# Performance work log

Hardware: AMD Instinct MI355X
Metric: run time of the kernel (lower is better)

The kernel has to match this reference:

```python
import jax, jax.numpy as jnp
import numpy as np

EPS = 1e-06  # min_gamma_value

def spectral_function(eigvals):
    # reciprocal spectral function: f(lambda) = 1 / lambda (lambda >= EPS by construction)
    return 1.0 / eigvals

def setup_inputs() -> dict:
    key = jax.random.key(0)
    x = jax.random.normal(key, (4, 64, 16, 128, 128), dtype=jnp.float32)  # [B, C, K, H, W]
    return {"x": x}

def reference(x):
    # [B, C, K, H, W] -> [B, H, W, K, C]
    m = jnp.transpose(x, (0, 3, 4, 2, 1))
    K = m.shape[-2]
    # per-pixel KxK Gram matrix, regularized
    sym = jnp.einsum('bhwkc,bhwlc->bhwkl', m, m) + EPS * jnp.eye(K, dtype=m.dtype)
    eigvals, eigvecs = jnp.linalg.eigh(sym)          # eigvals [B,H,W,K], eigvecs [B,H,W,K,K]
    f = spectral_function(eigvals)                    # elementwise spectral map
    # V diag(f) V^T
    out = jnp.einsum('bhwik,bhwk,bhwjk->bhwij', eigvecs, f, eigvecs)
    return out
```

## Files before the change

### kernel.cpp

```cpp
#include <hip/hip_runtime.h>
#include <utility>


#define EPSR 1e-6f
#define TS2 131

__device__ __host__ constexpr int rowof(int t) {
    int i = 0;
    while ((i + 1) * (i + 2) / 2 <= t) ++i;
    return i;
}
__device__ __host__ constexpr int colof(int t) { return t - rowof(t) * (rowof(t) + 1) / 2; }

__device__ __forceinline__ constexpr int tidx(int i, int j) {
    return i * (i + 1) / 2 + j;
}

#define GLOAD_LDS16(gp, lp)                                                       \
    __builtin_amdgcn_global_load_lds(                                             \
        (const __attribute__((address_space(1))) void*)(gp),                      \
        (__attribute__((address_space(3))) void*)(lp), 16, 0, 0)


template<int P>
__device__ __forceinline__ void fma_pair(const float (&m)[16], float& a) {
    a = fmaf(m[rowof(P)], m[colof(P)], a);
}

template<int G, int... TT>
__device__ __forceinline__ void fma_group(const float (&m)[16], float (&acc)[68],
                                          std::integer_sequence<int, TT...>) {
    (fma_pair<G * 68 + TT>(m, acc[TT]), ...);
}

template<int G>
__device__ __forceinline__ void chunk_fma2(const float* __restrict__ buf, int px,
                                           float (&acc)[68]) {
    #pragma unroll
    for (int cs = 0; cs < 2; ++cs) {
        float m[16];
        #pragma unroll
        for (int k = 0; k < 16; ++k) m[k] = buf[cs * 2048 + k * 128 + px];
        fma_group<G>(m, acc, std::make_integer_sequence<int, 68>{});
    }
}

template<int P>
__device__ __forceinline__ void store_tri_pair(float* __restrict__ tri, int px, float v) {
    constexpr bool diag = (rowof(P) == colof(P));
    tri[P * TS2 + px] = diag ? (v + EPSR) : v;
}

template<int G, int... TT>
__device__ __forceinline__ void store_tri_group(float* __restrict__ tri, int px,
                                                const float (&acc)[68],
                                                std::integer_sequence<int, TT...>) {
    (store_tri_pair<G * 68 + TT>(tri, px, acc[TT]), ...);
}


union SMem {
    float stage[2][4096];
    float tri[136 * TS2];
};

__global__ __launch_bounds__(256, 2)
void fused_gram_inv(const float* __restrict__ x, float* __restrict__ out) {
    __shared__ __align__(16) SMem sm;

    const int tid = threadIdx.x;
    const int lane = tid & 63;
    const int wv = tid >> 6;
    const int G = wv & 1;
    const int ph = wv >> 1;
    const int px = ph * 64 + lane;
    const int p0 = blockIdx.x * 128;
    const int b = blockIdx.x >> 7;
    const int hw0 = p0 & 16383;

    const float* gbase = x + (size_t)b * 16777216 + hw0
                           + (size_t)(lane >> 5) * 16384 + (size_t)(lane & 31) * 4;

    float acc[68];
    #pragma unroll
    for (int t = 0; t < 68; ++t) acc[t] = 0.0f;

    auto STAGE = [&](int bufi, int c0) {
        const float* gp = gbase + (size_t)(c0 + ph) * 262144
                                + (size_t)(G * 8) * 16384;
        #pragma unroll
        for (int q = 0; q < 4; ++q) {
            GLOAD_LDS16(gp + (size_t)(q * 2) * 16384,
                        &sm.stage[bufi][ph * 2048 + (G * 8 + q * 2) * 128]);
        }
    };

    STAGE(0, 0);
    for (int t = 0; t < 32; ++t) {
        __syncthreads();
        if (t < 31) STAGE((t + 1) & 1, 2 * (t + 1));
        const float* buf = sm.stage[t & 1];
        if (G == 0) chunk_fma2<0>(buf, px, acc);
        else        chunk_fma2<1>(buf, px, acc);
    }
    __syncthreads();

    if (G == 0) store_tri_group<0>(sm.tri, px, acc, std::make_integer_sequence<int, 68>{});
    else        store_tri_group<1>(sm.tri, px, acc, std::make_integer_sequence<int, 68>{});
    __syncthreads();

    if (G == 0) {
        float s[136];
        #pragma unroll
        for (int t = 0; t < 136; ++t) s[t] = sm.tri[t * TS2 + px];

        #pragma unroll
        for (int j = 0; j < 16; ++j) {
            float d = s[tidx(j, j)];
            #pragma unroll
            for (int q = 0; q < j; ++q) d = fmaf(-s[tidx(j, q)], s[tidx(j, q)], d);
            const float invd = 1.0f / sqrtf(d);
            s[tidx(j, j)] = invd;
            #pragma unroll
            for (int i = j + 1; i < 16; ++i) {
                float v = s[tidx(i, j)];
                #pragma unroll
                for (int q = 0; q < j; ++q) v = fmaf(-s[tidx(i, q)], s[tidx(j, q)], v);
                s[tidx(i, j)] = v * invd;
            }
        }

        #pragma unroll
        for (int j = 0; j < 16; ++j) {
            #pragma unroll
            for (int i = j + 1; i < 16; ++i) {
                float sum = s[tidx(i, j)] * s[tidx(j, j)];
                #pragma unroll
                for (int q = j + 1; q < i; ++q)
                    sum = fmaf(s[tidx(i, q)], s[tidx(q, j)], sum);
                s[tidx(i, j)] = -s[tidx(i, i)] * sum;
            }
        }

        #pragma unroll
        for (int j = 0; j < 16; ++j) {
            #pragma unroll
            for (int i = j; i < 16; ++i) {
                float sum = 0.0f;
                #pragma unroll
                for (int q = i; q < 16; ++q)
                    sum = fmaf(s[tidx(q, i)], s[tidx(q, j)], sum);
                s[tidx(i, j)] = sum;
            }
        }

        #pragma unroll
        for (int t = 0; t < 136; ++t) sm.tri[t * TS2 + px] = s[t];
    }
    __syncthreads();

    const int e = tid;
    const int i = e >> 4, j = e & 15;
    const int hi = i > j ? i : j;
    const int lo = i + j - hi;
    const int trow = hi * (hi + 1) / 2 + lo;
    float* gout = out + (size_t)p0 * 256;
    #pragma unroll 8
    for (int a = 0; a < 128; ++a) {
        gout[(size_t)a * 256 + e] = sm.tri[trow * TS2 + a];
    }
}

extern "C" void kernel_launch(void* const* d_in, const int* in_sizes, int n_in,
                              void* d_out, int out_size, void* d_ws, size_t ws_size,
                              hipStream_t stream) {
    const float* x = (const float*)d_in[0];
    float* out = (float*)d_out;
    hipLaunchKernelGGL(fused_gram_inv, dim3(512), dim3(256), 0, stream, x, out);
}
```

Measured before the change: 70.89 us.

## Use 512-thread blocks covering 256 pixels with single-channel staging

Each block now holds 512 threads and processes 256 pixels instead of 128, so the grid halves to 256 blocks. Each staging step loads one channel across 16 K-rows of 256 contiguous pixels, with 64 pipeline steps instead of 32. The triangle LDS stride grows to 259 to fit 256 pixels. The intent is longer contiguous global reads and less per-block overhead, at the cost of LDS use (136*259 floats, about 141KB), which allows only one block per CU, and of having only 256 blocks for the whole GPU.

```diff
diff --git a/kernel.cpp b/kernel.cpp
--- a/kernel.cpp
+++ b/kernel.cpp
@@ -3,7 +3,7 @@
 
 
 #define EPSR 1e-6f
-#define TS2 131
+#define TS3 259
 
 __device__ __host__ constexpr int rowof(int t) {
     int i = 0;
@@ -34,21 +34,18 @@
 }
 
 template<int G>
-__device__ __forceinline__ void chunk_fma2(const float* __restrict__ buf, int px,
+__device__ __forceinline__ void chunk_fma1(const float* __restrict__ buf, int px,
                                            float (&acc)[68]) {
+    float m[16];
     #pragma unroll
-    for (int cs = 0; cs < 2; ++cs) {
-        float m[16];
-        #pragma unroll
-        for (int k = 0; k < 16; ++k) m[k] = buf[cs * 2048 + k * 128 + px];
-        fma_group<G>(m, acc, std::make_integer_sequence<int, 68>{});
-    }
+    for (int k = 0; k < 16; ++k) m[k] = buf[k * 256 + px];
+    fma_group<G>(m, acc, std::make_integer_sequence<int, 68>{});
 }
 
 template<int P>
 __device__ __forceinline__ void store_tri_pair(float* __restrict__ tri, int px, float v) {
     constexpr bool diag = (rowof(P) == colof(P));
-    tri[P * TS2 + px] = diag ? (v + EPSR) : v;
+    tri[P * TS3 + px] = diag ? (v + EPSR) : v;
 }
 
 template<int G, int... TT>
@@ -61,10 +58,10 @@
 
 union SMem {
     float stage[2][4096];
-    float tri[136 * TS2];
+    float tri[136 * TS3];
 };
 
-__global__ __launch_bounds__(256, 2)
+__global__ __launch_bounds__(512, 2)
 void fused_gram_inv(const float* __restrict__ x, float* __restrict__ out) {
     __shared__ __align__(16) SMem sm;
 
@@ -74,34 +71,32 @@
     const int G = wv & 1;
     const int ph = wv >> 1;
     const int px = ph * 64 + lane;
-    const int p0 = blockIdx.x * 128;
-    const int b = blockIdx.x >> 7;
+    const int p0 = blockIdx.x * 256;
+    const int b = blockIdx.x >> 6;
     const int hw0 = p0 & 16383;
 
-    const float* gbase = x + (size_t)b * 16777216 + hw0
-                           + (size_t)(lane >> 5) * 16384 + (size_t)(lane & 31) * 4;
+    const float* gbase = x + (size_t)b * 16777216 + hw0 + (size_t)lane * 4;
 
     float acc[68];
     #pragma unroll
     for (int t = 0; t < 68; ++t) acc[t] = 0.0f;
 
-    auto STAGE = [&](int bufi, int c0) {
-        const float* gp = gbase + (size_t)(c0 + ph) * 262144
-                                + (size_t)(G * 8) * 16384;
+    auto STAGE = [&](int bufi, int c) {
+        const float* gp = gbase + (size_t)c * 262144;
         #pragma unroll
-        for (int q = 0; q < 4; ++q) {
-            GLOAD_LDS16(gp + (size_t)(q * 2) * 16384,
-                        &sm.stage[bufi][ph * 2048 + (G * 8 + q * 2) * 128]);
+        for (int q = 0; q < 2; ++q) {
+            const int k = wv * 2 + q;
+            GLOAD_LDS16(gp + (size_t)k * 16384, &sm.stage[bufi][k * 256]);
         }
     };
 
     STAGE(0, 0);
-    for (int t = 0; t < 32; ++t) {
+    for (int t = 0; t < 64; ++t) {
         __syncthreads();
-        if (t < 31) STAGE((t + 1) & 1, 2 * (t + 1));
+        if (t < 63) STAGE((t + 1) & 1, t + 1);
         const float* buf = sm.stage[t & 1];
-        if (G == 0) chunk_fma2<0>(buf, px, acc);
-        else        chunk_fma2<1>(buf, px, acc);
+        if (G == 0) chunk_fma1<0>(buf, px, acc);
+        else        chunk_fma1<1>(buf, px, acc);
     }
     __syncthreads();
 
@@ -112,7 +107,7 @@
     if (G == 0) {
         float s[136];
         #pragma unroll
-        for (int t = 0; t < 136; ++t) s[t] = sm.tri[t * TS2 + px];
+        for (int t = 0; t < 136; ++t) s[t] = sm.tri[t * TS3 + px];
 
         #pragma unroll
         for (int j = 0; j < 16; ++j) {
@@ -155,19 +150,20 @@
         }
 
         #pragma unroll
-        for (int t = 0; t < 136; ++t) sm.tri[t * TS2 + px] = s[t];
+        for (int t = 0; t < 136; ++t) sm.tri[t * TS3 + px] = s[t];
     }
     __syncthreads();
 
-    const int e = tid;
+    const int e = tid & 255;
+    const int half = tid >> 8;
     const int i = e >> 4, j = e & 15;
     const int hi = i > j ? i : j;
     const int lo = i + j - hi;
     const int trow = hi * (hi + 1) / 2 + lo;
     float* gout = out + (size_t)p0 * 256;
     #pragma unroll 8
-    for (int a = 0; a < 128; ++a) {
-        gout[(size_t)a * 256 + e] = sm.tri[trow * TS2 + a];
+    for (int a = half * 128; a < half * 128 + 128; ++a) {
+        gout[(size_t)a * 256 + e] = sm.tri[trow * TS3 + a];
     }
 }
 
@@ -176,5 +172,5 @@
                               hipStream_t stream) {
     const float* x = (const float*)d_in[0];
     float* out = (float*)d_out;
-    hipLaunchKernelGGL(fused_gram_inv, dim3(512), dim3(256), 0, stream, x, out);
+    hipLaunchKernelGGL(fused_gram_inv, dim3(256), dim3(512), 0, stream, x, out);
 }
```

Measured after the change: 77.36 us. 9.1% more time.
